# Performance work log

Measured on AMD Instinct MI355X. Metric: run time of the kernel, lower is better.

## Reference

```python
import jax, jax.numpy as jnp
import numpy as np

DT = 0.1
B_SZ = 8192
T_HIST = 20
LEN_PRED = 30
FEAT = 32
N_LAYERS = 3
# state transition for constant-acceleration model (matches self.F in torch)
F_MAT = np.array([[1.0, DT, DT * DT / 2], [0.0, 1.0, DT], [0.0, 0.0, 1.0]], dtype=np.float32)


def setup_inputs() -> dict:
    key = jax.random.key(0)
    ks = jax.random.split(key, 16)
    # random-walk trajectories as history observations
    hist = jnp.cumsum(jax.random.normal(ks[0], (B_SZ, T_HIST, 2), jnp.float32) * 0.5, axis=1)
    k_lin = 1.0 / np.sqrt(FEAT)
    k_in = 1.0 / np.sqrt(24)

    def u(k, shape, scale):
        return jax.random.uniform(k, shape, jnp.float32, -scale, scale)

    return {
        "hist": hist,
        "max_accel_x": jnp.ones((1,), jnp.float32) * 10.0,
        "max_accel_y": jnp.ones((1,), jnp.float32) * 20.0,
        "velocity_std_x": jnp.ones((1,), jnp.float32) * 10.0,
        "acceleration_std_x": jnp.ones((1,), jnp.float32) * 10.0,
        "R_x_": jnp.array([0.0448], jnp.float32),
        "R_y_": jnp.array([0.001], jnp.float32),
        "G_x": jnp.array([0.0059, 0.2981, 0.0393], jnp.float32),
        "G_y": jnp.array([0.0059, 0.2981, 0.0393], jnp.float32) / 5.0,
        "Win_W": u(ks[1], (FEAT, 24), k_in),
        "Win_b": u(ks[2], (FEAT,), k_in),
        "enc_Wih": u(ks[3], (N_LAYERS, 4 * FEAT, FEAT), k_lin),
        "enc_Whh": u(ks[4], (N_LAYERS, 4 * FEAT, FEAT), k_lin),
        "enc_bih": u(ks[5], (N_LAYERS, 4 * FEAT), k_lin),
        "enc_bhh": u(ks[6], (N_LAYERS, 4 * FEAT), k_lin),
        "dec_Wih": u(ks[7], (N_LAYERS, 4 * FEAT, FEAT), k_lin),
        "dec_Whh": u(ks[8], (N_LAYERS, 4 * FEAT, FEAT), k_lin),
        "dec_bih": u(ks[9], (N_LAYERS, 4 * FEAT), k_lin),
        "dec_bhh": u(ks[10], (N_LAYERS, 4 * FEAT), k_lin),
        "Wout_W": u(ks[11], (4, FEAT), k_lin),
        "Wout_b": u(ks[12], (4,), k_lin),
        "len_pred": LEN_PRED,
    }


def reference(hist, max_accel_x, max_accel_y, velocity_std_x, acceleration_std_x,
              R_x_, R_y_, G_x, G_y, Win_W, Win_b,
              enc_Wih, enc_Whh, enc_bih, enc_bhh,
              dec_Wih, dec_Whh, dec_bih, dec_bhh,
              Wout_W, Wout_b, len_pred):
    B = hist.shape[0]
    F = jnp.asarray(F_MAT)
    R_x = R_x_[0] * R_x_[0]
    R_y = R_y_[0] * R_y_[0]
    Z_x = hist[:, :, 0]
    Z_y = hist[:, :, 1]

    def lstm(x, h, c, Wih, Whh, bih, bhh):
        g = x @ Wih.T + bih + h @ Whh.T + bhh
        i, f, gg, o = jnp.split(g, 4, axis=1)
        c = jax.nn.sigmoid(f) * c + jax.nn.sigmoid(i) * jnp.tanh(gg)
        h = jax.nn.sigmoid(o) * jnp.tanh(c)
        return h, c

    def stack(XP, h, c, Wih, Whh, bih, bhh):
        x = jnp.tanh(XP @ Win_W.T + Win_b)
        hs, cs = [], []
        for j in range(N_LAYERS):
            hj, cj = lstm(x, h[j], c[j], Wih[j], Whh[j], bih[j], bhh[j])
            hs.append(hj)
            cs.append(cj)
            x = cj  # torch code feeds the fresh CELL state to the next layer
        return jnp.stack(hs), jnp.stack(cs)

    def kpred(X, P, Q):
        return X @ F.T, jnp.einsum('ij,bjk,lk->bil', F, P, F) + Q

    def kupdate(X, P, z, R):
        y = z - X[:, 0]                      # innovation (H picks component 0)
        S = P[:, 0, 0] + R                   # innovation covariance (scalar)
        K = P[:, :, 0] / S[:, None]          # Kalman gain (B,3)
        return X + y[:, None] * K, P - K[:, :, None] * P[:, 0:1, :]

    def kinit(z0):
        # torch always calls _kalman_init with is_x=True (default), so both
        # axes use R_x / velocity_std_x / acceleration_std_x
        X = jnp.zeros((B, 3), hist.dtype).at[:, 0].set(z0)
        d = jnp.stack([R_x, velocity_std_x[0] ** 2, acceleration_std_x[0] ** 2])
        P = jnp.zeros((B, 3, 3), hist.dtype).at[:, jnp.arange(3), jnp.arange(3)].set(d)
        return X, P

    Qx_e = jnp.outer(G_x * max_accel_x[0], G_x * max_accel_x[0])
    Qy_e = jnp.outer(G_y * max_accel_y[0], G_y * max_accel_y[0])

    Xx, Px = kinit(Z_x[:, 0])
    Xy, Py = kinit(Z_y[:, 0])
    h = jnp.zeros((N_LAYERS, B, FEAT), hist.dtype)
    c = jnp.zeros_like(h)

    def enc_step(carry, zs):
        Xx, Px, Xy, Py, h, c = carry
        zx, zy = zs
        XP = jnp.concatenate([Xx, Xy, Px.reshape(B, 9), Py.reshape(B, 9)], 1)
        h, c = stack(XP, h, c, enc_Wih, enc_Whh, enc_bih, enc_bhh)
        Xx, Px = kpred(Xx, Px, Qx_e)
        Xy, Py = kpred(Xy, Py, Qy_e)
        Xx, Px = kupdate(Xx, Px, zx, R_x)
        Xy, Py = kupdate(Xy, Py, zy, R_y)
        return (Xx, Px, Xy, Py, h, c), None

    carry, _ = jax.lax.scan(enc_step, (Xx, Px, Xy, Py, h, c),
                            (Z_x[:, 1:].T, Z_y[:, 1:].T))

    oxx = jnp.outer(G_x, G_x)
    oyy = jnp.outer(G_y, G_y)

    def dec_step(carry, _):
        Xx, Px, Xy, Py, h, c = carry
        XP = jnp.concatenate([Xx, Xy, Px.reshape(B, 9), Py.reshape(B, 9)], 1)
        h, c = stack(XP, h, c, dec_Wih, dec_Whh, dec_bih, dec_bhh)
        pred = c[-1] @ Wout_W.T + Wout_b  # (B,4): [u_x, u_y, std_x, std_y]
        Xx = Xx.at[:, 2].set(DT * pred[:, 0])  # X[:,2] = B*u
        Xy = Xy.at[:, 2].set(DT * pred[:, 1])
        Qx = (pred[:, 2] ** 2)[:, None, None] * oxx
        Qy = (pred[:, 3] ** 2)[:, None, None] * oyy
        Xx, Px = kpred(Xx, Px, Qx)
        Xy, Py = kpred(Xy, Py, Qy)
        out = jnp.stack([Xx[:, 0], Xy[:, 0],
                         jnp.sqrt(Px[:, 0, 0]), jnp.sqrt(Py[:, 0, 0]),
                         jnp.zeros(B, hist.dtype)], axis=1)  # (B,5)
        return (Xx, Px, Xy, Py, h, c), out

    carry, ys = jax.lax.scan(dec_step, carry, None, length=len_pred)
    return jnp.transpose(ys, (1, 0, 2))  # (B, len_pred, 5)
```

## Files before the change

kernel.cpp:

```cpp
#include <hip/hip_runtime.h>
#include <math.h>

#define DT   0.1f
#define HDT  0.005f
#define T_HIST 20
#define LEN_PRED 30

typedef __attribute__((ext_vector_type(8))) short bfrag8;
typedef __attribute__((ext_vector_type(4))) short short4v;
typedef __attribute__((ext_vector_type(4))) float f32x4;

#define WS_FRAG   0u
#define WS_WIN    98304u
#define WS_WOUT   100352u
#define WS_BIAS   101376u

static __device__ __forceinline__ unsigned short f2bf(float x) {
    union { float f; unsigned int u; } v; v.f = x;
    unsigned int r = v.u + 0x7fffu + ((v.u >> 16) & 1u);
    return (unsigned short)(r >> 16);
}

__global__ void prep_kernel(const float* __restrict__ Win_W,
                            const float* __restrict__ eWih, const float* __restrict__ eWhh,
                            const float* __restrict__ ebih, const float* __restrict__ ebhh,
                            const float* __restrict__ dWih, const float* __restrict__ dWhh,
                            const float* __restrict__ dbih, const float* __restrict__ dbhh,
                            const float* __restrict__ Wout_W,
                            char* __restrict__ ws)
{
    int i = blockIdx.x * blockDim.x + threadIdx.x;
    if (i < 49152) {
        int fi = i >> 9, within = i & 511;
        int lane = within >> 3, jj = within & 7;
        int c = fi & 1, j = (fi >> 1) & 1, wvv = (fi >> 2) & 3;
        int pl = fi >> 4;
        int l = pl % 3, ph = pl / 3;
        int m = lane & 15, q2 = lane >> 4;
        int gate = m & 3;
        int feat = wvv * 8 + 4 * j + (m >> 2);
        int row = gate * 32 + feat;
        int k = q2 * 8 + jj;
        const float* W = (c == 0) ? (ph ? dWih : eWih) : (ph ? dWhh : eWhh);
        ((unsigned short*)(ws + WS_FRAG))[i] = f2bf(W[l * 4096 + row * 32 + k]);
    } else if (i < 50176) {
        int i2 = i - 49152;
        int w = i2 >> 9, within = i2 & 511;
        int lane = within >> 3, jj = within & 7;
        int m = lane & 15, q2 = lane >> 4;
        int k = q2 * 8 + jj;
        float v = (k < 24) ? Win_W[(w * 16 + m) * 24 + k] : 0.f;
        ((unsigned short*)(ws + WS_WIN))[i2] = f2bf(v);
    } else if (i < 50688) {
        int i3 = i - 50176;
        int lane = i3 >> 3, jj = i3 & 7;
        int m = lane & 15, q2 = lane >> 4;
        float v = (m < 4) ? Wout_W[m * 32 + q2 * 8 + jj] : 0.f;
        ((unsigned short*)(ws + WS_WOUT))[i3] = f2bf(v);
    } else if (i < 51456) {
        int b = i - 50688;
        int ph = b / 384, rem = b % 384;
        int l = rem >> 7, row = rem & 127;
        const float* bi = ph ? dbih : ebih;
        const float* bh = ph ? dbhh : ebhh;
        ((float*)(ws + WS_BIAS))[b] = bi[l * 128 + row] + bh[l * 128 + row];
    }
}

__launch_bounds__(256, 2)
__global__ void kalman_lstm_kernel(const float* __restrict__ hist,
                                   const float* __restrict__ max_ax, const float* __restrict__ max_ay,
                                   const float* __restrict__ vstd, const float* __restrict__ astd,
                                   const float* __restrict__ Rx_, const float* __restrict__ Ry_,
                                   const float* __restrict__ Gx, const float* __restrict__ Gy,
                                   const float* __restrict__ Win_b, const float* __restrict__ Wout_b,
                                   const char* __restrict__ ws, float* __restrict__ out)
{
    __shared__ __align__(16) unsigned short xin[4][16][40];
    __shared__ __align__(16) unsigned short hbuf[2][3][16][40];
    __shared__ __align__(16) unsigned short xpw[2][16][40];

    const int tid  = threadIdx.x;
    const int wv   = tid >> 6;
    const int lane = tid & 63;
    const int q    = lane >> 4;
    const int m    = lane & 15;
    const int b_elem = blockIdx.x * 16 + m;

    bfrag8 fragA[3][2][2];
    float  biasR[3][2][4];
    const bfrag8* fragp = (const bfrag8*)(ws + WS_FRAG);
    const float*  combp = (const float*)(ws + WS_BIAS);
    auto load_phase = [&](int ph) {
#pragma unroll
        for (int l = 0; l < 3; ++l)
#pragma unroll
            for (int j = 0; j < 2; ++j) {
#pragma unroll
                for (int c = 0; c < 2; ++c) {
                    int fi = (((ph * 3 + l) * 4 + wv) * 2 + j) * 2 + c;
                    fragA[l][j][c] = fragp[fi * 64 + lane];
                }
#pragma unroll
                for (int r = 0; r < 4; ++r)
                    biasR[l][j][r] = combp[ph * 384 + l * 128 + r * 32 + (wv * 8 + 4 * j + q)];
            }
    };
    load_phase(0);

    bfrag8 winF = {}, woutF = {};
    f32x4 winB = {0.f, 0.f, 0.f, 0.f};
    float wb0 = 0.f, wb1 = 0.f, wb2 = 0.f, wb3 = 0.f;
    float g0 = 0.f, g1 = 0.f, g2 = 0.f, ge0 = 0.f, ge1 = 0.f, ge2 = 0.f;
    float Rch = 0.f, X0 = 0.f, X1 = 0.f, X2 = 0.f;
    float P00 = 0.f, P01 = 0.f, P02 = 0.f, P11 = 0.f, P12 = 0.f, P22 = 0.f;
    const int ch = q & 1;
    if (wv >= 2) {
        int w = wv - 2;
        winF  = ((const bfrag8*)(ws + WS_WIN))[w * 64 + lane];
        woutF = ((const bfrag8*)(ws + WS_WOUT))[lane];
#pragma unroll
        for (int r = 0; r < 4; ++r) winB[r] = Win_b[w * 16 + q * 4 + r];
        wb0 = Wout_b[0]; wb1 = Wout_b[1]; wb2 = Wout_b[2]; wb3 = Wout_b[3];
        const float rx = Rx_[0] * Rx_[0], ry = Ry_[0] * Ry_[0];
        Rch = ch ? ry : rx;
        if (ch == 0) { g0 = Gx[0]; g1 = Gx[1]; g2 = Gx[2]; float s = max_ax[0]; ge0 = g0*s; ge1 = g1*s; ge2 = g2*s; }
        else         { g0 = Gy[0]; g1 = Gy[1]; g2 = Gy[2]; float s = max_ay[0]; ge0 = g0*s; ge1 = g1*s; ge2 = g2*s; }
        X0 = hist[b_elem * (T_HIST * 2) + ch];
        P00 = Rch; P11 = vstd[0] * vstd[0]; P22 = astd[0] * astd[0];
    }

    float creg[3][2];
#pragma unroll
    for (int l = 0; l < 3; ++l) { creg[l][0] = 0.f; creg[l][1] = 0.f; }

    for (int idx = tid; idx < 4 * 16 * 40; idx += 256) (&xin[0][0][0])[idx] = 0;
    for (int idx = tid; idx < 2 * 3 * 16 * 40; idx += 256) (&hbuf[0][0][0][0])[idx] = 0;
    for (int idx = tid; idx < 2 * 16 * 40; idx += 256) (&xpw[0][0][0])[idx] = 0;

    auto sig = [](float z) { return __builtin_amdgcn_rcpf(1.f + __expf(-z)); };
    auto th  = [](float z) { return fmaf(-2.f, __builtin_amdgcn_rcpf(__expf(2.f * z) + 1.f), 1.f); };

    auto kpred = [&](float Q00, float Q01, float Q02, float Q11, float Q12, float Q22) {
        X0 = X0 + DT * X1 + HDT * X2;
        X1 = X1 + DT * X2;
        float M00 = P00 + DT * P01 + HDT * P02;
        float M01 = P01 + DT * P11 + HDT * P12;
        float M02 = P02 + DT * P12 + HDT * P22;
        float M11 = P11 + DT * P12;
        float M12 = P12 + DT * P22;
        float M22 = P22;
        P00 = M00 + DT * M01 + HDT * M02 + Q00;
        P01 = M01 + DT * M02 + Q01;
        P02 = M02 + Q02;
        P11 = M11 + DT * M12 + Q11;
        P12 = M12 + Q12;
        P22 = M22 + Q22;
    };
    auto kupdate = [&](float z) {
        float y = z - X0;
        float Sinv = 1.0f / (P00 + Rch);
        float K0 = P00 * Sinv, K1 = P01 * Sinv, K2 = P02 * Sinv;
        X0 += y * K0; X1 += y * K1; X2 += y * K2;
        float p00 = P00, p01 = P01, p02 = P02;
        P00 = p00 - K0 * p00;
        P01 = p01 - K0 * p01;
        P02 = p02 - K0 * p02;
        P11 = P11 - K1 * p01;
        P12 = P12 - K1 * p02;
        P22 = P22 - K2 * p02;
    };
    auto write_xp = [&]() {
        if (q < 2) {
            unsigned short* row = &xpw[wv - 2][m][0];
            int o = ch * 3;
            row[o + 0] = f2bf(X0); row[o + 1] = f2bf(X1); row[o + 2] = f2bf(X2);
            int pb = 6 + ch * 9;
            row[pb + 0] = f2bf(P00); row[pb + 1] = f2bf(P01); row[pb + 2] = f2bf(P02);
            row[pb + 3] = f2bf(P01); row[pb + 4] = f2bf(P11); row[pb + 5] = f2bf(P12);
            row[pb + 6] = f2bf(P02); row[pb + 7] = f2bf(P12); row[pb + 8] = f2bf(P22);
        }
    };

    const f32x4 zero4 = {0.f, 0.f, 0.f, 0.f};

    auto regionA = [&](int mode, int t) {
        if (wv >= 2) {
            if (mode == 0) {
                if (t > 0) {
                    float z = hist[b_elem * (T_HIST * 2) + t * 2 + ch];
                    kpred(ge0 * ge0, ge0 * ge1, ge0 * ge2, ge1 * ge1, ge1 * ge2, ge2 * ge2);
                    kupdate(z);
                }
            } else {
                if (t == 0) {
                    float z = hist[b_elem * (T_HIST * 2) + 19 * 2 + ch];
                    kpred(ge0 * ge0, ge0 * ge1, ge0 * ge2, ge1 * ge1, ge1 * ge2, ge2 * ge2);
                    kupdate(z);
                } else {
                    bfrag8 bc2 = *(const bfrag8*)&xin[3][m][q * 8];
                    f32x4 ap = __builtin_amdgcn_mfma_f32_16x16x32_bf16(woutF, bc2, zero4, 0, 0, 0);
                    float a0 = ap[0] + wb0, a1 = ap[1] + wb1, a2 = ap[2] + wb2, a3 = ap[3] + wb3;
                    float s0 = __shfl(a0, m), s1 = __shfl(a1, m);
                    float s2 = __shfl(a2, m), s3 = __shfl(a3, m);
                    float pe = ch ? s1 : s0;
                    float qe = ch ? s3 : s2;
                    X2 = DT * pe;
                    float qs = qe * qe;
                    kpred(qs*g0*g0, qs*g0*g1, qs*g0*g2, qs*g1*g1, qs*g1*g2, qs*g2*g2);
                    if (wv == 2 && q < 2) {
                        float* o = out + (size_t)b_elem * (LEN_PRED * 5) + (t - 1) * 5;
                        if (ch == 0) { o[0] = X0; o[2] = sqrtf(P00); }
                        else         { o[1] = X0; o[3] = sqrtf(P00); o[4] = 0.f; }
                    }
                }
            }
            write_xp();
            bfrag8 bxp = *(const bfrag8*)&xpw[wv - 2][m][q * 8];
            f32x4 aw = __builtin_amdgcn_mfma_f32_16x16x32_bf16(winF, bxp, zero4, 0, 0, 0);
            union { short4v v; unsigned short s[4]; } u;
#pragma unroll
            for (int r = 0; r < 4; ++r) u.s[r] = f2bf(th(aw[r] + winB[r]));
            *(short4v*)&xin[0][m][(wv - 2) * 16 + q * 4] = u.v;
        }
        __syncthreads();
    };

    auto layers = [&](int p) {
#pragma unroll
        for (int l = 0; l < 3; ++l) {
            bfrag8 bx = *(const bfrag8*)&xin[l][m][q * 8];
            bfrag8 bh = *(const bfrag8*)&hbuf[p][l][m][q * 8];
            f32x4 a0 = __builtin_amdgcn_mfma_f32_16x16x32_bf16(fragA[l][0][0], bx, zero4, 0, 0, 0);
            a0        = __builtin_amdgcn_mfma_f32_16x16x32_bf16(fragA[l][0][1], bh, a0, 0, 0, 0);
            f32x4 a1 = __builtin_amdgcn_mfma_f32_16x16x32_bf16(fragA[l][1][0], bx, zero4, 0, 0, 0);
            a1        = __builtin_amdgcn_mfma_f32_16x16x32_bf16(fragA[l][1][1], bh, a1, 0, 0, 0);
#pragma unroll
            for (int j = 0; j < 2; ++j) {
                f32x4 a = j ? a1 : a0;
                float iv = sig(a[0] + biasR[l][j][0]);
                float fv = sig(a[1] + biasR[l][j][1]);
                float gv = th (a[2] + biasR[l][j][2]);
                float ov = sig(a[3] + biasR[l][j][3]);
                float cn = fmaf(fv, creg[l][j], iv * gv);
                float hn = ov * th(cn);
                creg[l][j] = cn;
                int f = wv * 8 + 4 * j + q;
                xin[l + 1][m][f] = f2bf(cn);
                hbuf[p ^ 1][l][m][f] = f2bf(hn);
            }
            __syncthreads();
        }
    };

    __syncthreads();
    int p = 0;

    for (int t = 0; t < T_HIST - 1; ++t) { regionA(0, t); layers(p); p ^= 1; }
    load_phase(1);
    for (int t = 0; t < LEN_PRED; ++t)   { regionA(1, t); layers(p); p ^= 1; }

    if (wv == 2) {
        bfrag8 bc2 = *(const bfrag8*)&xin[3][m][q * 8];
        f32x4 ap = __builtin_amdgcn_mfma_f32_16x16x32_bf16(woutF, bc2, zero4, 0, 0, 0);
        float a0 = ap[0] + wb0, a1 = ap[1] + wb1, a2 = ap[2] + wb2, a3 = ap[3] + wb3;
        float s0 = __shfl(a0, m), s1 = __shfl(a1, m);
        float s2 = __shfl(a2, m), s3 = __shfl(a3, m);
        float pe = ch ? s1 : s0;
        float qe = ch ? s3 : s2;
        X2 = DT * pe;
        float qs = qe * qe;
        kpred(qs*g0*g0, qs*g0*g1, qs*g0*g2, qs*g1*g1, qs*g1*g2, qs*g2*g2);
        if (q < 2) {
            float* o = out + (size_t)b_elem * (LEN_PRED * 5) + (LEN_PRED - 1) * 5;
            if (ch == 0) { o[0] = X0; o[2] = sqrtf(P00); }
            else         { o[1] = X0; o[3] = sqrtf(P00); o[4] = 0.f; }
        }
    }
}

extern "C" void kernel_launch(void* const* d_in, const int* in_sizes, int n_in,
                              void* d_out, int out_size, void* d_ws, size_t ws_size,
                              hipStream_t stream)
{
    const float* hist  = (const float*)d_in[0];
    const float* maxax = (const float*)d_in[1];
    const float* maxay = (const float*)d_in[2];
    const float* vstd  = (const float*)d_in[3];
    const float* astd  = (const float*)d_in[4];
    const float* Rx    = (const float*)d_in[5];
    const float* Ry    = (const float*)d_in[6];
    const float* Gx    = (const float*)d_in[7];
    const float* Gy    = (const float*)d_in[8];
    const float* WinW  = (const float*)d_in[9];
    const float* Winb  = (const float*)d_in[10];
    const float* eWih  = (const float*)d_in[11];
    const float* eWhh  = (const float*)d_in[12];
    const float* ebih  = (const float*)d_in[13];
    const float* ebhh  = (const float*)d_in[14];
    const float* dWih  = (const float*)d_in[15];
    const float* dWhh  = (const float*)d_in[16];
    const float* dbih  = (const float*)d_in[17];
    const float* dbhh  = (const float*)d_in[18];
    const float* WoutW = (const float*)d_in[19];
    const float* Woutb = (const float*)d_in[20];
    char* ws = (char*)d_ws;
    float* out = (float*)d_out;

    prep_kernel<<<202, 256, 0, stream>>>(WinW, eWih, eWhh, ebih, ebhh,
                                         dWih, dWhh, dbih, dbhh, WoutW, ws);
    kalman_lstm_kernel<<<512, 256, 0, stream>>>(hist, maxax, maxay, vstd, astd,
                                                Rx, Ry, Gx, Gy, Winb, Woutb,
                                                ws, out);
}
```

Measured before the change: 193.9 us.

## Run each 16-element tile on a single wave with register-resident LSTM state

Replaces the four-wave block (with LDS exchange and __syncthreads between layers) by one 64-lane wave per 16 batch elements. All gate weights for each layer stay in registers, and h/c are passed between layers as packed bf16 MFMA fragments instead of through shared memory. The prep kernel folds the log2e scaling and bias into the weights, so the activations become a single exp2 plus rcp, and the bias rides in the MFMA accumulator. This removes block-level barriers but makes each wave's serial MFMA chain much longer, and the large register footprint limits how many waves fit per CU.

```diff
diff --git a/kernel.cpp b/kernel.cpp
--- a/kernel.cpp
+++ b/kernel.cpp
@@ -5,15 +5,18 @@
 #define HDT  0.005f
 #define T_HIST 20
 #define LEN_PRED 30
+#define NLOG2E   (-1.4426950408889634f)
+#define TWOLOG2E ( 2.8853900817779268f)
 
 typedef __attribute__((ext_vector_type(8))) short bfrag8;
-typedef __attribute__((ext_vector_type(4))) short short4v;
 typedef __attribute__((ext_vector_type(4))) float f32x4;
 
-#define WS_FRAG   0u
-#define WS_WIN    98304u
-#define WS_WOUT   100352u
-#define WS_BIAS   101376u
+#define WS_FRAG  0u
+#define WS_WIN   98304u
+#define WS_WOUT  100352u
+#define WS_BIASC 101376u
+#define WS_WINC  102912u
+#define WS_WOUTB 103040u
 
 static __device__ __forceinline__ unsigned short f2bf(float x) {
     union { float f; unsigned int u; } v; v.f = x;
@@ -21,125 +24,134 @@
     return (unsigned short)(r >> 16);
 }
 
-__global__ void prep_kernel(const float* __restrict__ Win_W,
+static __device__ __forceinline__ unsigned int pack2bf(float lo, float hi) {
+    unsigned int ul = __float_as_uint(lo) + 0x8000u;
+    unsigned int uh = __float_as_uint(hi) + 0x8000u;
+    return __builtin_amdgcn_perm(uh, ul, 0x07060302u);
+}
+
+static __device__ __forceinline__ float rcp1(float z) {
+    return __builtin_amdgcn_rcpf(1.f + __builtin_amdgcn_exp2f(z));
+}
+static __device__ __forceinline__ float th_(float z) {
+    return fmaf(-2.f, rcp1(z), 1.f);
+}
+
+__global__ void prep_kernel(const float* __restrict__ Win_W, const float* __restrict__ Win_b,
                             const float* __restrict__ eWih, const float* __restrict__ eWhh,
                             const float* __restrict__ ebih, const float* __restrict__ ebhh,
                             const float* __restrict__ dWih, const float* __restrict__ dWhh,
                             const float* __restrict__ dbih, const float* __restrict__ dbhh,
-                            const float* __restrict__ Wout_W,
+                            const float* __restrict__ Wout_W, const float* __restrict__ Wout_b,
                             char* __restrict__ ws)
 {
     int i = blockIdx.x * blockDim.x + threadIdx.x;
     if (i < 49152) {
-        int fi = i >> 9, within = i & 511;
-        int lane = within >> 3, jj = within & 7;
-        int c = fi & 1, j = (fi >> 1) & 1, wvv = (fi >> 2) & 3;
-        int pl = fi >> 4;
+        int fi = i >> 9, w = i & 511;
+        int lane = w >> 3, jj = w & 7;
+        int c = fi & 1, j = (fi >> 1) & 7, pl = fi >> 4;
         int l = pl % 3, ph = pl / 3;
-        int m = lane & 15, q2 = lane >> 4;
-        int gate = m & 3;
-        int feat = wvv * 8 + 4 * j + (m >> 2);
-        int row = gate * 32 + feat;
-        int k = q2 * 8 + jj;
-        const float* W = (c == 0) ? (ph ? dWih : eWih) : (ph ? dWhh : eWhh);
-        ((unsigned short*)(ws + WS_FRAG))[i] = f2bf(W[l * 4096 + row * 32 + k]);
+        int mm = lane & 15, qq = lane >> 4;
+        int gate = mm & 3;
+        int row = gate * 32 + 8 * (mm >> 2) + j;
+        int k = qq * 8 + jj;
+        float scale = (gate == 2) ? TWOLOG2E : NLOG2E;
+        const float* W = c ? (ph ? dWhh : eWhh) : (ph ? dWih : eWih);
+        ((unsigned short*)(ws + WS_FRAG))[i] = f2bf(W[l * 4096 + row * 32 + k] * scale);
     } else if (i < 50176) {
         int i2 = i - 49152;
-        int w = i2 >> 9, within = i2 & 511;
-        int lane = within >> 3, jj = within & 7;
-        int m = lane & 15, q2 = lane >> 4;
-        int k = q2 * 8 + jj;
-        float v = (k < 24) ? Win_W[(w * 16 + m) * 24 + k] : 0.f;
+        int T = i2 >> 9, w = i2 & 511;
+        int lane = w >> 3, jj = w & 7;
+        int mm = lane & 15, qq = lane >> 4;
+        int feat = 8 * (mm >> 2) + 4 * T + (mm & 3);
+        int k = qq * 8 + jj;
+        float v = (k < 24) ? Win_W[feat * 24 + k] * TWOLOG2E : 0.f;
         ((unsigned short*)(ws + WS_WIN))[i2] = f2bf(v);
     } else if (i < 50688) {
         int i3 = i - 50176;
         int lane = i3 >> 3, jj = i3 & 7;
-        int m = lane & 15, q2 = lane >> 4;
-        float v = (m < 4) ? Wout_W[m * 32 + q2 * 8 + jj] : 0.f;
+        int mm = lane & 15, qq = lane >> 4;
+        float v = (mm < 4) ? Wout_W[mm * 32 + qq * 8 + jj] : 0.f;
         ((unsigned short*)(ws + WS_WOUT))[i3] = f2bf(v);
-    } else if (i < 51456) {
+    } else if (i < 51072) {
         int b = i - 50688;
-        int ph = b / 384, rem = b % 384;
-        int l = rem >> 7, row = rem & 127;
+        int r = b & 3, qq = (b >> 2) & 3, j = (b >> 4) & 7, pl = b >> 7;
+        int l = pl % 3, ph = pl / 3;
+        int row = r * 32 + 8 * qq + j;
+        float scale = (r == 2) ? TWOLOG2E : NLOG2E;
         const float* bi = ph ? dbih : ebih;
         const float* bh = ph ? dbhh : ebhh;
-        ((float*)(ws + WS_BIAS))[b] = bi[l * 128 + row] + bh[l * 128 + row];
+        ((float*)(ws + WS_BIASC))[b] = (bi[l * 128 + row] + bh[l * 128 + row]) * scale;
+    } else if (i < 51104) {
+        int b = i - 51072;
+        int r = b & 3, qq = (b >> 2) & 3, T = b >> 4;
+        ((float*)(ws + WS_WINC))[b] = Win_b[8 * qq + 4 * T + r] * TWOLOG2E;
+    } else if (i < 51108) {
+        ((float*)(ws + WS_WOUTB))[i - 51104] = Wout_b[i - 51104];
     }
 }
 
-__launch_bounds__(256, 2)
+__launch_bounds__(64)
 __global__ void kalman_lstm_kernel(const float* __restrict__ hist,
                                    const float* __restrict__ max_ax, const float* __restrict__ max_ay,
                                    const float* __restrict__ vstd, const float* __restrict__ astd,
                                    const float* __restrict__ Rx_, const float* __restrict__ Ry_,
                                    const float* __restrict__ Gx, const float* __restrict__ Gy,
-                                   const float* __restrict__ Win_b, const float* __restrict__ Wout_b,
                                    const char* __restrict__ ws, float* __restrict__ out)
 {
-    __shared__ __align__(16) unsigned short xin[4][16][40];
-    __shared__ __align__(16) unsigned short hbuf[2][3][16][40];
-    __shared__ __align__(16) unsigned short xpw[2][16][40];
-
-    const int tid  = threadIdx.x;
-    const int wv   = tid >> 6;
-    const int lane = tid & 63;
-    const int q    = lane >> 4;
-    const int m    = lane & 15;
+    __shared__ unsigned short xp[16][40];
+
+    const int lane = threadIdx.x;
+    const int q = lane >> 4, m = lane & 15, ch = q & 1;
     const int b_elem = blockIdx.x * 16 + m;
 
-    bfrag8 fragA[3][2][2];
-    float  biasR[3][2][4];
+    for (int i = lane; i < 640; i += 64) (&xp[0][0])[i] = 0;
+    __builtin_amdgcn_wave_barrier();
+
+    bfrag8 fragA[3][8][2];
+    f32x4  biasC[3][8];
     const bfrag8* fragp = (const bfrag8*)(ws + WS_FRAG);
-    const float*  combp = (const float*)(ws + WS_BIAS);
+    const f32x4*  biasp = (const f32x4*)(ws + WS_BIASC);
     auto load_phase = [&](int ph) {
 #pragma unroll
         for (int l = 0; l < 3; ++l)
 #pragma unroll
-            for (int j = 0; j < 2; ++j) {
-#pragma unroll
-                for (int c = 0; c < 2; ++c) {
-                    int fi = (((ph * 3 + l) * 4 + wv) * 2 + j) * 2 + c;
-                    fragA[l][j][c] = fragp[fi * 64 + lane];
-                }
-#pragma unroll
-                for (int r = 0; r < 4; ++r)
-                    biasR[l][j][r] = combp[ph * 384 + l * 128 + r * 32 + (wv * 8 + 4 * j + q)];
+            for (int j = 0; j < 8; ++j) {
+#pragma unroll
+                for (int c = 0; c < 2; ++c)
+                    fragA[l][j][c] = fragp[(((ph * 3 + l) * 8 + j) * 2 + c) * 64 + lane];
+                biasC[l][j] = biasp[((ph * 3 + l) * 8 + j) * 4 + q];
             }
     };
     load_phase(0);
 
-    bfrag8 winF = {}, woutF = {};
-    f32x4 winB = {0.f, 0.f, 0.f, 0.f};
-    float wb0 = 0.f, wb1 = 0.f, wb2 = 0.f, wb3 = 0.f;
-    float g0 = 0.f, g1 = 0.f, g2 = 0.f, ge0 = 0.f, ge1 = 0.f, ge2 = 0.f;
-    float Rch = 0.f, X0 = 0.f, X1 = 0.f, X2 = 0.f;
-    float P00 = 0.f, P01 = 0.f, P02 = 0.f, P11 = 0.f, P12 = 0.f, P22 = 0.f;
-    const int ch = q & 1;
-    if (wv >= 2) {
-        int w = wv - 2;
-        winF  = ((const bfrag8*)(ws + WS_WIN))[w * 64 + lane];
-        woutF = ((const bfrag8*)(ws + WS_WOUT))[lane];
-#pragma unroll
-        for (int r = 0; r < 4; ++r) winB[r] = Win_b[w * 16 + q * 4 + r];
-        wb0 = Wout_b[0]; wb1 = Wout_b[1]; wb2 = Wout_b[2]; wb3 = Wout_b[3];
-        const float rx = Rx_[0] * Rx_[0], ry = Ry_[0] * Ry_[0];
-        Rch = ch ? ry : rx;
-        if (ch == 0) { g0 = Gx[0]; g1 = Gx[1]; g2 = Gx[2]; float s = max_ax[0]; ge0 = g0*s; ge1 = g1*s; ge2 = g2*s; }
-        else         { g0 = Gy[0]; g1 = Gy[1]; g2 = Gy[2]; float s = max_ay[0]; ge0 = g0*s; ge1 = g1*s; ge2 = g2*s; }
-        X0 = hist[b_elem * (T_HIST * 2) + ch];
-        P00 = Rch; P11 = vstd[0] * vstd[0]; P22 = astd[0] * astd[0];
-    }
-
-    float creg[3][2];
-#pragma unroll
-    for (int l = 0; l < 3; ++l) { creg[l][0] = 0.f; creg[l][1] = 0.f; }
-
-    for (int idx = tid; idx < 4 * 16 * 40; idx += 256) (&xin[0][0][0])[idx] = 0;
-    for (int idx = tid; idx < 2 * 3 * 16 * 40; idx += 256) (&hbuf[0][0][0][0])[idx] = 0;
-    for (int idx = tid; idx < 2 * 16 * 40; idx += 256) (&xpw[0][0][0])[idx] = 0;
-
-    auto sig = [](float z) { return __builtin_amdgcn_rcpf(1.f + __expf(-z)); };
-    auto th  = [](float z) { return fmaf(-2.f, __builtin_amdgcn_rcpf(__expf(2.f * z) + 1.f), 1.f); };
+    bfrag8 winF0 = ((const bfrag8*)(ws + WS_WIN))[lane];
+    bfrag8 winF1 = ((const bfrag8*)(ws + WS_WIN))[64 + lane];
+    f32x4  winC0 = ((const f32x4*)(ws + WS_WINC))[q];
+    f32x4  winC1 = ((const f32x4*)(ws + WS_WINC))[4 + q];
+    bfrag8 woutF = ((const bfrag8*)(ws + WS_WOUT))[lane];
+    const float* wbp = (const float*)(ws + WS_WOUTB);
+    const float wb0 = wbp[0], wb1 = wbp[1], wb2 = wbp[2], wb3 = wbp[3];
+
+    const float rx = Rx_[0] * Rx_[0], ry = Ry_[0] * Ry_[0];
+    const float Rch = ch ? ry : rx;
+    float g0, g1, g2, s;
+    if (ch == 0) { g0 = Gx[0]; g1 = Gx[1]; g2 = Gx[2]; s = max_ax[0]; }
+    else         { g0 = Gy[0]; g1 = Gy[1]; g2 = Gy[2]; s = max_ay[0]; }
+    const float ge0 = g0 * s, ge1 = g1 * s, ge2 = g2 * s;
+    float X0 = (q < 2) ? hist[b_elem * 40 + ch] : 0.f;
+    float X1 = 0.f, X2 = 0.f;
+    float P00 = Rch, P01 = 0.f, P02 = 0.f;
+    float P11 = vstd[0] * vstd[0], P12 = 0.f, P22 = astd[0] * astd[0];
+
+    union { unsigned int u[4]; bfrag8 v; } zf; zf.u[0] = zf.u[1] = zf.u[2] = zf.u[3] = 0;
+    bfrag8 hfrag[3] = { zf.v, zf.v, zf.v };
+    float cst[3][8];
+#pragma unroll
+    for (int l = 0; l < 3; ++l)
+#pragma unroll
+        for (int j = 0; j < 8; ++j) cst[l][j] = 0.f;
+    bfrag8 xfrag = zf.v;
 
     auto kpred = [&](float Q00, float Q01, float Q02, float Q11, float Q12, float Q22) {
         X0 = X0 + DT * X1 + HDT * X2;
@@ -170,9 +182,10 @@
         P12 = P12 - K1 * p02;
         P22 = P22 - K2 * p02;
     };
-    auto write_xp = [&]() {
+
+    auto stack = [&]() {
         if (q < 2) {
-            unsigned short* row = &xpw[wv - 2][m][0];
+            unsigned short* row = &xp[m][0];
             int o = ch * 3;
             row[o + 0] = f2bf(X0); row[o + 1] = f2bf(X1); row[o + 2] = f2bf(X2);
             int pb = 6 + ch * 9;
@@ -180,99 +193,78 @@
             row[pb + 3] = f2bf(P01); row[pb + 4] = f2bf(P11); row[pb + 5] = f2bf(P12);
             row[pb + 6] = f2bf(P02); row[pb + 7] = f2bf(P12); row[pb + 8] = f2bf(P22);
         }
-    };
-
-    const f32x4 zero4 = {0.f, 0.f, 0.f, 0.f};
-
-    auto regionA = [&](int mode, int t) {
-        if (wv >= 2) {
-            if (mode == 0) {
-                if (t > 0) {
-                    float z = hist[b_elem * (T_HIST * 2) + t * 2 + ch];
-                    kpred(ge0 * ge0, ge0 * ge1, ge0 * ge2, ge1 * ge1, ge1 * ge2, ge2 * ge2);
-                    kupdate(z);
+        __builtin_amdgcn_wave_barrier();
+        bfrag8 bxp = *(const bfrag8*)&xp[m][q * 8];
+        __builtin_amdgcn_wave_barrier();
+        f32x4 t0 = __builtin_amdgcn_mfma_f32_16x16x32_bf16(winF0, bxp, winC0, 0, 0, 0);
+        f32x4 t1 = __builtin_amdgcn_mfma_f32_16x16x32_bf16(winF1, bxp, winC1, 0, 0, 0);
+        union { unsigned int u[4]; bfrag8 v; } xu;
+        xu.u[0] = pack2bf(th_(t0[0]), th_(t0[1]));
+        xu.u[1] = pack2bf(th_(t0[2]), th_(t0[3]));
+        xu.u[2] = pack2bf(th_(t1[0]), th_(t1[1]));
+        xu.u[3] = pack2bf(th_(t1[2]), th_(t1[3]));
+        xfrag = xu.v;
+#pragma unroll
+        for (int l = 0; l < 3; ++l) {
+            f32x4 acc[8];
+#pragma unroll
+            for (int j = 0; j < 8; ++j) {
+                f32x4 hh = __builtin_amdgcn_mfma_f32_16x16x32_bf16(fragA[l][j][1], hfrag[l], biasC[l][j], 0, 0, 0);
+                acc[j]   = __builtin_amdgcn_mfma_f32_16x16x32_bf16(fragA[l][j][0], xfrag, hh, 0, 0, 0);
+            }
+            union { unsigned int u[4]; bfrag8 v; } xu2, hu2;
+#pragma unroll
+            for (int jp = 0; jp < 4; ++jp) {
+                float cn[2], hn[2];
+#pragma unroll
+                for (int e = 0; e < 2; ++e) {
+                    int j = jp * 2 + e;
+                    float iv = rcp1(acc[j][0]);
+                    float fv = rcp1(acc[j][1]);
+                    float gv = th_(acc[j][2]);
+                    float ov = rcp1(acc[j][3]);
+                    float cv = fmaf(fv, cst[l][j], iv * gv);
+                    cst[l][j] = cv;
+                    float tc = th_(cv * TWOLOG2E);
+                    cn[e] = cv; hn[e] = ov * tc;
                 }
-            } else {
-                if (t == 0) {
-                    float z = hist[b_elem * (T_HIST * 2) + 19 * 2 + ch];
-                    kpred(ge0 * ge0, ge0 * ge1, ge0 * ge2, ge1 * ge1, ge1 * ge2, ge2 * ge2);
-                    kupdate(z);
-                } else {
-                    bfrag8 bc2 = *(const bfrag8*)&xin[3][m][q * 8];
-                    f32x4 ap = __builtin_amdgcn_mfma_f32_16x16x32_bf16(woutF, bc2, zero4, 0, 0, 0);
-                    float a0 = ap[0] + wb0, a1 = ap[1] + wb1, a2 = ap[2] + wb2, a3 = ap[3] + wb3;
-                    float s0 = __shfl(a0, m), s1 = __shfl(a1, m);
-                    float s2 = __shfl(a2, m), s3 = __shfl(a3, m);
-                    float pe = ch ? s1 : s0;
-                    float qe = ch ? s3 : s2;
-                    X2 = DT * pe;
-                    float qs = qe * qe;
-                    kpred(qs*g0*g0, qs*g0*g1, qs*g0*g2, qs*g1*g1, qs*g1*g2, qs*g2*g2);
-                    if (wv == 2 && q < 2) {
-                        float* o = out + (size_t)b_elem * (LEN_PRED * 5) + (t - 1) * 5;
-                        if (ch == 0) { o[0] = X0; o[2] = sqrtf(P00); }
-                        else         { o[1] = X0; o[3] = sqrtf(P00); o[4] = 0.f; }
-                    }
-                }
+                xu2.u[jp] = pack2bf(cn[0], cn[1]);
+                hu2.u[jp] = pack2bf(hn[0], hn[1]);
             }
-            write_xp();
-            bfrag8 bxp = *(const bfrag8*)&xpw[wv - 2][m][q * 8];
-            f32x4 aw = __builtin_amdgcn_mfma_f32_16x16x32_bf16(winF, bxp, zero4, 0, 0, 0);
-            union { short4v v; unsigned short s[4]; } u;
-#pragma unroll
-            for (int r = 0; r < 4; ++r) u.s[r] = f2bf(th(aw[r] + winB[r]));
-            *(short4v*)&xin[0][m][(wv - 2) * 16 + q * 4] = u.v;
-        }
-        __syncthreads();
-    };
-
-    auto layers = [&](int p) {
-#pragma unroll
-        for (int l = 0; l < 3; ++l) {
-            bfrag8 bx = *(const bfrag8*)&xin[l][m][q * 8];
-            bfrag8 bh = *(const bfrag8*)&hbuf[p][l][m][q * 8];
-            f32x4 a0 = __builtin_amdgcn_mfma_f32_16x16x32_bf16(fragA[l][0][0], bx, zero4, 0, 0, 0);
-            a0        = __builtin_amdgcn_mfma_f32_16x16x32_bf16(fragA[l][0][1], bh, a0, 0, 0, 0);
-            f32x4 a1 = __builtin_amdgcn_mfma_f32_16x16x32_bf16(fragA[l][1][0], bx, zero4, 0, 0, 0);
-            a1        = __builtin_amdgcn_mfma_f32_16x16x32_bf16(fragA[l][1][1], bh, a1, 0, 0, 0);
-#pragma unroll
-            for (int j = 0; j < 2; ++j) {
-                f32x4 a = j ? a1 : a0;
-                float iv = sig(a[0] + biasR[l][j][0]);
-                float fv = sig(a[1] + biasR[l][j][1]);
-                float gv = th (a[2] + biasR[l][j][2]);
-                float ov = sig(a[3] + biasR[l][j][3]);
-                float cn = fmaf(fv, creg[l][j], iv * gv);
-                float hn = ov * th(cn);
-                creg[l][j] = cn;
-                int f = wv * 8 + 4 * j + q;
-                xin[l + 1][m][f] = f2bf(cn);
-                hbuf[p ^ 1][l][m][f] = f2bf(hn);
-            }
-            __syncthreads();
+            xfrag = xu2.v;
+            hfrag[l] = hu2.v;
         }
     };
 
-    __syncthreads();
-    int p = 0;
-
-    for (int t = 0; t < T_HIST - 1; ++t) { regionA(0, t); layers(p); p ^= 1; }
+    const f32x4 zero4 = {0.f, 0.f, 0.f, 0.f};
+
+    float znext = (q < 2) ? hist[b_elem * 40 + 2 + ch] : 0.f;
+#pragma unroll 1
+    for (int t = 0; t < T_HIST - 1; ++t) {
+        stack();
+        float z = znext;
+        if (t < 18) znext = (q < 2) ? hist[b_elem * 40 + (t + 2) * 2 + ch] : 0.f;
+        kpred(ge0 * ge0, ge0 * ge1, ge0 * ge2, ge1 * ge1, ge1 * ge2, ge2 * ge2);
+        kupdate(z);
+    }
+
     load_phase(1);
-    for (int t = 0; t < LEN_PRED; ++t)   { regionA(1, t); layers(p); p ^= 1; }
-
-    if (wv == 2) {
-        bfrag8 bc2 = *(const bfrag8*)&xin[3][m][q * 8];
-        f32x4 ap = __builtin_amdgcn_mfma_f32_16x16x32_bf16(woutF, bc2, zero4, 0, 0, 0);
-        float a0 = ap[0] + wb0, a1 = ap[1] + wb1, a2 = ap[2] + wb2, a3 = ap[3] + wb3;
-        float s0 = __shfl(a0, m), s1 = __shfl(a1, m);
-        float s2 = __shfl(a2, m), s3 = __shfl(a3, m);
+
+#pragma unroll 1
+    for (int t = 0; t < LEN_PRED; ++t) {
+        stack();
+        f32x4 ap = __builtin_amdgcn_mfma_f32_16x16x32_bf16(woutF, xfrag, zero4, 0, 0, 0);
+        float s0 = __shfl(ap[0] + wb0, m);
+        float s1 = __shfl(ap[1] + wb1, m);
+        float s2 = __shfl(ap[2] + wb2, m);
+        float s3 = __shfl(ap[3] + wb3, m);
         float pe = ch ? s1 : s0;
         float qe = ch ? s3 : s2;
         X2 = DT * pe;
         float qs = qe * qe;
-        kpred(qs*g0*g0, qs*g0*g1, qs*g0*g2, qs*g1*g1, qs*g1*g2, qs*g2*g2);
+        kpred(qs * g0 * g0, qs * g0 * g1, qs * g0 * g2, qs * g1 * g1, qs * g1 * g2, qs * g2 * g2);
         if (q < 2) {
-            float* o = out + (size_t)b_elem * (LEN_PRED * 5) + (LEN_PRED - 1) * 5;
+            float* o = out + (size_t)b_elem * (LEN_PRED * 5) + t * 5;
             if (ch == 0) { o[0] = X0; o[2] = sqrtf(P00); }
             else         { o[1] = X0; o[3] = sqrtf(P00); o[4] = 0.f; }
         }
@@ -307,9 +299,8 @@
     char* ws = (char*)d_ws;
     float* out = (float*)d_out;
 
-    prep_kernel<<<202, 256, 0, stream>>>(WinW, eWih, eWhh, ebih, ebhh,
-                                         dWih, dWhh, dbih, dbhh, WoutW, ws);
-    kalman_lstm_kernel<<<512, 256, 0, stream>>>(hist, maxax, maxay, vstd, astd,
-                                                Rx, Ry, Gx, Gy, Winb, Woutb,
-                                                ws, out);
-}
+    prep_kernel<<<200, 256, 0, stream>>>(WinW, Winb, eWih, eWhh, ebih, ebhh,
+                                         dWih, dWhh, dbih, dbhh, WoutW, Woutb, ws);
+    kalman_lstm_kernel<<<512, 64, 0, stream>>>(hist, maxax, maxay, vstd, astd,
+                                               Rx, Ry, Gx, Gy, ws, out);
+}
```

Result: slower. 217.1 us (+12.0%).
